# Kernel tuning notes

Measured on AMD Instinct MI355X. Metric: run time of the kernel, lower is better.

The kernel has to match this reference:

```python
import jax, jax.numpy as jnp
import numpy as np

TS = 16      # tile size
ST = 4       # stride
IN = 224     # image size
G = (IN - TS) // ST + 1   # 53 tiles per side
L = G * G                 # 2809 tiles
CH = [3 * L, 3 * L // 4, 3 * L // 16, 3 * L // 4, 3 * L]  # [8427,2106,526,2106,8427]

# torch_dct-style unnormalized DCT-II matrix and its exact inverse (DCT-III based)
_n = np.arange(TS)
_k = np.arange(TS)[:, None]
_C = np.cos(np.pi * (2 * _n[None, :] + 1) * _k / (2 * TS))  # [k, n]
D_DCT = jnp.asarray(2.0 * _C, jnp.float32)                   # dct: y = D @ x
_w = np.ones(TS); _w[0] = 0.5
D_IDCT = jnp.asarray((_C.T * _w[None, :]) / TS, jnp.float32) # idct: x = Dinv @ y

# gather/scatter indices for unfold/fold (constants)
IH = (np.arange(G) * ST)[:, None] + np.arange(TS)[None, :]   # [G, TS]
IW = IH


def setup_inputs() -> dict:
    key = jax.random.key(0)
    ks = jax.random.split(key, 9)
    x = jax.random.normal(ks[0], (8, 3, IN, IN), jnp.float32)
    def lin(k, o, c):
        return jax.random.normal(k, (o, c), jnp.float32) * 0.02
    return {
        'x': x,
        'w1': lin(ks[1], CH[1], CH[0]), 'b1': jnp.zeros((CH[1],), jnp.float32),
        'w2': lin(ks[2], CH[2], CH[1]), 'b2': jnp.zeros((CH[2],), jnp.float32),
        'w3': lin(ks[3], CH[3], CH[2]), 'b3': jnp.zeros((CH[3],), jnp.float32),
        'w4': lin(ks[4], CH[4], CH[3]), 'b4': jnp.zeros((CH[4],), jnp.float32),
    }


def _forward(x, w1, b1, w2, b2, w3, b3, w4, b4):
    b = x.shape[0]
    # unfold: gather overlapping 16x16 patches -> [b, 3, G, G, TS, TS]
    p = x[:, :, IH[:, None, :, None], IW[None, :, None, :]]
    # torch ordering after permute+reshape: channel index = l*3 + c
    tiles = p.transpose(0, 2, 3, 1, 4, 5).reshape(b, 3 * L, TS, TS)
    # 2D DCT (unnormalized DCT-II along last two dims)
    dct_tiles = jnp.einsum('km,ln,bcmn->bckl', D_DCT, D_DCT, tiles)
    # mask net: stack of 1x1 convs over the tile-channel dim
    h = dct_tiles / (TS * TS)
    h = jax.nn.relu(jnp.einsum('oc,bchw->bohw', w1, h) + b1[:, None, None])
    h = jax.nn.relu(jnp.einsum('oc,bchw->bohw', w2, h) + b2[:, None, None])
    h = jax.nn.relu(jnp.einsum('oc,bchw->bohw', w3, h) + b3[:, None, None])
    masks = jax.nn.sigmoid(jnp.einsum('oc,bchw->bohw', w4, h) + b4[:, None, None])
    clean_dct = masks * dct_tiles
    # 2D inverse DCT
    clean_tiles = jnp.einsum('mk,nl,bckl->bcmn', D_IDCT, D_IDCT, clean_dct)
    # fold: scatter-add patches back with overlap
    ct = clean_tiles.reshape(b, G, G, 3, TS, TS).transpose(0, 3, 1, 2, 4, 5)
    out = jnp.zeros((b, 3, IN, IN), x.dtype)
    out = out.at[:, :, IH[:, None, :, None], IW[None, :, None, :]].add(ct)
    # scale = fold(unfold(ones)): per-pixel overlap counts (recomputed per call, as in source)
    scale = jnp.zeros((IN, IN), x.dtype)
    scale = scale.at[IH[:, None, :, None], IW[None, :, None, :]].add(
        jnp.ones((G, G, TS, TS), x.dtype))
    return out / scale


def reference(x, w1, b1, w2, b2, w3, b3, w4, b4):
    return _forward(x, w1, b1, w2, b2, w3, b3, w4, b4)
```

## Files before the change

### kernel.cpp

```cpp
#include <hip/hip_runtime.h>
#include <stdint.h>

constexpr int INSZ = 224;
constexpr int GD   = 53;
constexpr int C0R = 8427, C1R = 2106, C2R = 526;
constexpr int C0P = 8448, C1P = 2304, C2P = 640;
constexpr int NTOK = 2048;

typedef __attribute__((ext_vector_type(4))) float f32x4;
typedef __attribute__((ext_vector_type(8))) short bf16x8;

constexpr float CT[64] = {
  1.00000000f,  0.99518473f,  0.98078528f,  0.95694034f,
  0.92387953f,  0.88192126f,  0.83146961f,  0.77301045f,
  0.70710678f,  0.63439328f,  0.55557023f,  0.47139674f,
  0.38268343f,  0.29028468f,  0.19509032f,  0.09801714f,
  0.00000000f, -0.09801714f, -0.19509032f, -0.29028468f,
 -0.38268343f, -0.47139674f, -0.55557023f, -0.63439328f,
 -0.70710678f, -0.77301045f, -0.83146961f, -0.88192126f,
 -0.92387953f, -0.95694034f, -0.98078528f, -0.99518473f,
 -1.00000000f, -0.99518473f, -0.98078528f, -0.95694034f,
 -0.92387953f, -0.88192126f, -0.83146961f, -0.77301045f,
 -0.70710678f, -0.63439328f, -0.55557023f, -0.47139674f,
 -0.38268343f, -0.29028468f, -0.19509032f, -0.09801714f,
 -0.00000000f,  0.09801714f,  0.19509032f,  0.29028468f,
  0.38268343f,  0.47139674f,  0.55557023f,  0.63439328f,
  0.70710678f,  0.77301045f,  0.83146961f,  0.88192126f,
  0.92387953f,  0.95694034f,  0.98078528f,  0.99518473f
};
constexpr float Dfwd(int k, int n) { return 2.0f * CT[((2 * n + 1) * k) & 63]; }
constexpr float Dinv(int n, int k) { return CT[((2 * n + 1) * k) & 63] * (k == 0 ? 0.03125f : 0.0625f); }

constexpr int TRS_R = 20, TRS_T = 336;
constexpr int TRS_SZ = 15 * TRS_T + 15 * TRS_R + 16;

__device__ __forceinline__ unsigned short f2bf(float f) {
  union { float f; unsigned u; } v; v.f = f;
  return (unsigned short)((v.u + 0x7FFFu + ((v.u >> 16) & 1u)) >> 16);
}
__device__ __forceinline__ float bf2f(unsigned short b) {
  union { unsigned u; float f; } v; v.u = ((unsigned)b) << 16;
  return v.f;
}

__device__ __forceinline__ void gload_lds16(const void* g, void* l) {
  __builtin_amdgcn_global_load_lds(
      (__attribute__((address_space(1))) unsigned int*)(uintptr_t)g,
      (__attribute__((address_space(3))) unsigned int*)(unsigned int)(uintptr_t)l,
      16, 0, 0);
}

__device__ __forceinline__ void xcd_tile(int& bx, int& by) {
  const int gx = gridDim.x, gy = gridDim.y;
  const int nwg = gx * gy;
  const int bid = blockIdx.y * gx + blockIdx.x;
  const int cpx = nwg >> 3;
  const int l = (bid & 7) * cpx + (bid >> 3);
  const int stripe = gy << 2;
  const int bxg = l / stripe;
  const int r = l - bxg * stripe;
  const int rem = gx - (bxg << 2);
  const int w = rem < 4 ? rem : 4;
  by = r / w;
  bx = (bxg << 2) + (r - by * w);
}

constexpr int CV1_GPR = C0P / 8;
constexpr int CV1_TOT = C1P * CV1_GPR;
__global__ __launch_bounds__(256)
void cvt_pad8_w1(const float* __restrict__ src, unsigned short* __restrict__ dst) {
  const int i = blockIdx.x * 256 + threadIdx.x;
  if (i >= CV1_TOT) return;
  const int m = i / CV1_GPR;
  const int k0 = (i - m * CV1_GPR) * 8;
  const float* sr = src + (size_t)m * C0R + k0;
  const bool mok = (m < C1R);
  unsigned short h[8];
#pragma unroll
  for (int e = 0; e < 8; ++e)
    h[e] = f2bf((mok && k0 + e < C0R) ? sr[e] : 0.f);
  uint4 pk;
  pk.x = (unsigned)h[0] | ((unsigned)h[1] << 16);
  pk.y = (unsigned)h[2] | ((unsigned)h[3] << 16);
  pk.z = (unsigned)h[4] | ((unsigned)h[5] << 16);
  pk.w = (unsigned)h[6] | ((unsigned)h[7] << 16);
  *(uint4*)&dst[(size_t)m * C0P + k0] = pk;
}

constexpr int CV8_1 = C2P * C1P / 8;
constexpr int CV8_2 = CV8_1 + C1P * C2P / 8;
constexpr int CV8_T = CV8_2 + C0P * C1P / 8;
__global__ __launch_bounds__(256)
void cvt_pad8_all(const float* __restrict__ w2, const float* __restrict__ w3,
                  const float* __restrict__ w4, unsigned short* __restrict__ d2,
                  unsigned short* __restrict__ d3, unsigned short* __restrict__ d4) {
  const int i = blockIdx.x * 256 + threadIdx.x;
  const float* src; unsigned short* dst;
  int m, k0, Kreal, Mreal, Kp;
  if (i < CV8_1) {
    const int gpr = C1P / 8;
    m = i / gpr; k0 = (i - m * gpr) * 8;
    src = w2; dst = d2; Mreal = C2R; Kreal = C1R; Kp = C1P;
  } else if (i < CV8_2) {
    const int j = i - CV8_1;
    const int gpr = C2P / 8;
    m = j / gpr; k0 = (j - m * gpr) * 8;
    src = w3; dst = d3; Mreal = C1R; Kreal = C2R; Kp = C2P;
  } else {
    const int j = i - CV8_2;
    const int gpr = C1P / 8;
    m = j / gpr; k0 = (j - m * gpr) * 8;
    src = w4; dst = d4; Mreal = C0R; Kreal = C1R; Kp = C1P;
  }
  const float* sr = src + (size_t)m * Kreal + k0;
  const bool mok = (m < Mreal);
  unsigned short h[8];
#pragma unroll
  for (int e = 0; e < 8; ++e)
    h[e] = f2bf((mok && k0 + e < Kreal) ? sr[e] : 0.f);
  uint4 pk;
  pk.x = (unsigned)h[0] | ((unsigned)h[1] << 16);
  pk.y = (unsigned)h[2] | ((unsigned)h[3] << 16);
  pk.z = (unsigned)h[4] | ((unsigned)h[5] << 16);
  pk.w = (unsigned)h[6] | ((unsigned)h[7] << 16);
  *(uint4*)&dst[(size_t)m * Kp + k0] = pk;
}

__global__ __launch_bounds__(256)
void dct_h0(const float* __restrict__ x, unsigned short* __restrict__ H0) {
  __shared__ float trp[TRS_SZ];
  __shared__ unsigned short hst[256 * 64];
  const int tid = threadIdx.x;
  const int b   = blockIdx.y;
  const int c0  = blockIdx.x * 64;
  const int t = tid >> 4, q = tid & 15;

  for (int g = 0; g < 4; ++g) {
    const int c = c0 + g * 16 + t;
    float p[16];
    {
      float4 v0{}, v1{}, v2{}, v3{};
      if (c < C0R) {
        const int ch = c % 3, gw = (c / 3) % GD, gh = c / (3 * GD);
        const float* xr = x + ((size_t)(b * 3 + ch) * INSZ + (gh * 4 + q)) * INSZ + gw * 4;
        v0 = *(const float4*)(xr);      v1 = *(const float4*)(xr + 4);
        v2 = *(const float4*)(xr + 8);  v3 = *(const float4*)(xr + 12);
      }
      p[0]=v0.x; p[1]=v0.y; p[2]=v0.z; p[3]=v0.w;
      p[4]=v1.x; p[5]=v1.y; p[6]=v1.z; p[7]=v1.w;
      p[8]=v2.x; p[9]=v2.y; p[10]=v2.z; p[11]=v2.w;
      p[12]=v3.x; p[13]=v3.y; p[14]=v3.z; p[15]=v3.w;
    }
    float r[16];
#pragma unroll
    for (int k = 0; k < 16; ++k) {
      float s = 0.f;
#pragma unroll
      for (int n = 0; n < 16; ++n) s += p[n] * Dfwd(k, n);
      r[k] = s;
    }
    float* wr = &trp[t * TRS_T + q * TRS_R];
#pragma unroll
    for (int k = 0; k < 16; k += 4)
      *(float4*)(wr + k) = make_float4(r[k], r[k+1], r[k+2], r[k+3]);
    __syncthreads();
    const int j = q;
    float rr[16];
#pragma unroll
    for (int i = 0; i < 16; ++i) rr[i] = trp[t * TRS_T + i * TRS_R + j];
#pragma unroll
    for (int k = 0; k < 16; ++k) {
      float s = 0.f;
#pragma unroll
      for (int i = 0; i < 16; ++i) s += rr[i] * Dfwd(k, i);
      hst[(k * 16 + j) * 64 + g * 16 + t] = f2bf(s * (1.f / 256.f));
    }
    __syncthreads();
  }
  const size_t base = ((size_t)b * 256) * C0P + c0;
#pragma unroll
  for (int i = 0; i < 8; ++i) {
    const int s = i * 256 + tid;
    const int kl = s >> 3, c16 = s & 7;
    *(uint4*)&H0[base + (size_t)kl * C0P + c16 * 8] = *(const uint4*)&hst[kl * 64 + c16 * 8];
  }
}

template<int ACT, int OUT_NM, int SPLITK>
__global__ __launch_bounds__(512, 2)
void gemm256(const unsigned short* __restrict__ W, const unsigned short* __restrict__ Ht,
             const float* __restrict__ bias, void* __restrict__ outp,
             int ldo, int Kp, int chunkK) {
  __shared__ unsigned short As[4][8192];
  __shared__ unsigned short Bs[4][8192];
  int bx, by; xcd_tile(bx, by);
  const int m0 = bx * 256, n0 = by * 256;
  const int tid = threadIdx.x;
  const int w = tid >> 6, lane = tid & 63;
  const int wr = w >> 2, wc = w & 3;
  const int lhi = lane >> 4, llo = lane & 15;
  const int kbase = SPLITK ? blockIdx.z * chunkK : 0;
  const int nkt = chunkK >> 5;

  const int srow = tid >> 2;
  const int slgc = ((tid & 3) ^ ((srow >> 1) & 3)) * 8;

  f32x4 acc[8][4];
#pragma unroll
  for (int i = 0; i < 8; ++i)
#pragma unroll
    for (int j = 0; j < 4; ++j) acc[i][j] = f32x4{0.f, 0.f, 0.f, 0.f};

  auto STAGE_A = [&](int kt, int buf) {
    const int kb = kbase + kt * 32 + slgc;
    gload_lds16(W + (size_t)(m0 + srow) * Kp + kb,       &As[buf][w * 512]);
    gload_lds16(W + (size_t)(m0 + 128 + srow) * Kp + kb, &As[buf][4096 + w * 512]);
  };
  auto STAGE_B = [&](int kt, int buf) {
    const int kb = kbase + kt * 32 + slgc;
    gload_lds16(Ht + (size_t)(n0 + srow) * Kp + kb,       &Bs[buf][w * 512]);
    gload_lds16(Ht + (size_t)(n0 + 128 + srow) * Kp + kb, &Bs[buf][4096 + w * 512]);
  };

  STAGE_A(0, 0); STAGE_B(0, 0);
  if (nkt > 1) { STAGE_A(1, 1); STAGE_B(1, 1); }
  if (nkt > 2) { STAGE_A(2, 2); STAGE_B(2, 2); }
  if (nkt > 2)      asm volatile("s_waitcnt vmcnt(8)" ::: "memory");
  else if (nkt > 1) asm volatile("s_waitcnt vmcnt(4)" ::: "memory");
  else              asm volatile("s_waitcnt vmcnt(0)" ::: "memory");
  __builtin_amdgcn_s_barrier();

  for (int kt = 0; kt < nkt; ++kt) {
    const int buf  = kt & 3;
    const int sbuf = (kt + 3) & 3;
    bf16x8 af[4], bfr[4];
#pragma unroll
    for (int mi = 0; mi < 4; ++mi) {
      const int row = wr * 128 + mi * 16 + llo;
      af[mi] = *(const bf16x8*)(&As[buf][row * 32 + ((lhi ^ ((row >> 1) & 3)) << 3)]);
    }
#pragma unroll
    for (int ni = 0; ni < 4; ++ni) {
      const int row = wc * 64 + ni * 16 + llo;
      bfr[ni] = *(const bf16x8*)(&Bs[buf][row * 32 + ((lhi ^ ((row >> 1) & 3)) << 3)]);
    }
    if (kt + 3 < nkt) STAGE_A(kt + 3, sbuf);
    __builtin_amdgcn_s_barrier();
    asm volatile("s_waitcnt lgkmcnt(0)" ::: "memory");
    __builtin_amdgcn_sched_barrier(0);
    __builtin_amdgcn_s_setprio(1);
#pragma unroll
    for (int mi = 0; mi < 4; ++mi)
#pragma unroll
      for (int ni = 0; ni < 4; ++ni)
        acc[mi][ni] = OUT_NM
          ? __builtin_amdgcn_mfma_f32_16x16x32_bf16(bfr[ni], af[mi], acc[mi][ni], 0, 0, 0)
          : __builtin_amdgcn_mfma_f32_16x16x32_bf16(af[mi], bfr[ni], acc[mi][ni], 0, 0, 0);
    __builtin_amdgcn_s_setprio(0);
    __builtin_amdgcn_s_barrier();
#pragma unroll
    for (int mi = 0; mi < 4; ++mi) {
      const int row = wr * 128 + 64 + mi * 16 + llo;
      af[mi] = *(const bf16x8*)(&As[buf][row * 32 + ((lhi ^ ((row >> 1) & 3)) << 3)]);
    }
    if (kt + 3 < nkt) STAGE_B(kt + 3, sbuf);
    __builtin_amdgcn_s_barrier();
    asm volatile("s_waitcnt lgkmcnt(0)" ::: "memory");
    __builtin_amdgcn_sched_barrier(0);
    __builtin_amdgcn_s_setprio(1);
#pragma unroll
    for (int mi = 0; mi < 4; ++mi)
#pragma unroll
      for (int ni = 0; ni < 4; ++ni)
        acc[4 + mi][ni] = OUT_NM
          ? __builtin_amdgcn_mfma_f32_16x16x32_bf16(bfr[ni], af[mi], acc[4 + mi][ni], 0, 0, 0)
          : __builtin_amdgcn_mfma_f32_16x16x32_bf16(af[mi], bfr[ni], acc[4 + mi][ni], 0, 0, 0);
    __builtin_amdgcn_s_setprio(0);
    if (kt + 1 < nkt) {
      if (kt + 4 <= nkt)      asm volatile("s_waitcnt vmcnt(8)" ::: "memory");
      else if (kt + 3 == nkt) asm volatile("s_waitcnt vmcnt(4)" ::: "memory");
      else                    asm volatile("s_waitcnt vmcnt(0)" ::: "memory");
    }
    __builtin_amdgcn_s_barrier();
  }

  if (SPLITK) {
    float* pz = (float*)outp + (size_t)blockIdx.z * ((size_t)NTOK * ldo);
#pragma unroll
    for (int mh = 0; mh < 2; ++mh)
#pragma unroll
      for (int mi = 0; mi < 4; ++mi) {
        const int mg = m0 + wr * 128 + mh * 64 + mi * 16 + llo;
#pragma unroll
        for (int ni = 0; ni < 4; ++ni) {
          const int ng = n0 + wc * 64 + ni * 16 + lhi * 4;
#pragma unroll
          for (int r = 0; r < 4; ++r)
            pz[(size_t)(ng + r) * ldo + mg] = acc[mh * 4 + mi][ni][r];
        }
      }
  } else {
    unsigned short* out = (unsigned short*)outp;
#pragma unroll
    for (int mh = 0; mh < 2; ++mh)
#pragma unroll
      for (int mi = 0; mi < 4; ++mi) {
        const int mgb = m0 + wr * 128 + mh * 64 + mi * 16 + lhi * 4;
#pragma unroll
        for (int ni = 0; ni < 4; ++ni) {
          const int ng = n0 + wc * 64 + ni * 16 + llo;
#pragma unroll
          for (int r = 0; r < 4; ++r) {
            const int mg = mgb + r;
            float v = acc[mh * 4 + mi][ni][r] + bias[mg];
            if (ACT == 1) v = fmaxf(v, 0.f);
            else if (ACT == 2) v = 1.f / (1.f + expf(-v));
            out[(size_t)mg * ldo + ng] = f2bf(v);
          }
        }
      }
  }
}

template<int OUT_NM>
__device__ __forceinline__ void gemm_core(
    const unsigned short* __restrict__ W, const unsigned short* __restrict__ Ht,
    unsigned short (*As)[128 * 32], unsigned short (*Bs)[128 * 32],
    int m0, int n0, int Kp, int kbase, int nkt, int w, int lane, f32x4 acc[4][4]) {
  const int wr = w >> 1, wc = w & 1;
  const int lhi = lane >> 4, llo = lane & 15;

  const int chunk0 = w * 64 + lane;
  const int row0 = chunk0 >> 2, kc0 = chunk0 & 3;
  const int kcg0 = kc0 ^ ((row0 >> 1) & 3);
  const int chunk1 = 256 + w * 64 + lane;
  const int row1 = chunk1 >> 2, kc1 = chunk1 & 3;
  const int kcg1 = kc1 ^ ((row1 >> 1) & 3);

  auto STAGE = [&](int kt, int sel) {
    const int kb = kbase + kt * 32;
    gload_lds16(W  + (size_t)(m0 + row0) * Kp + kb + kcg0 * 8, &As[sel][(w * 64) * 8]);
    gload_lds16(Ht + (size_t)(n0 + row0) * Kp + kb + kcg0 * 8, &Bs[sel][(w * 64) * 8]);
    gload_lds16(W  + (size_t)(m0 + row1) * Kp + kb + kcg1 * 8, &As[sel][(256 + w * 64) * 8]);
    gload_lds16(Ht + (size_t)(n0 + row1) * Kp + kb + kcg1 * 8, &Bs[sel][(256 + w * 64) * 8]);
  };

  STAGE(0, 0);
  if (nkt > 1) STAGE(1, 1);

  int cur = 0, nxt = 1, nx2 = 2;
  for (int kt = 0; kt < nkt; ++kt) {
    if (kt + 1 < nkt) {
      asm volatile("s_waitcnt vmcnt(4)" ::: "memory");
      __builtin_amdgcn_s_barrier();
      __builtin_amdgcn_sched_barrier(0);
      if (kt + 2 < nkt) STAGE(kt + 2, nx2);
    } else {
      asm volatile("s_waitcnt vmcnt(0)" ::: "memory");
      __builtin_amdgcn_s_barrier();
      __builtin_amdgcn_sched_barrier(0);
    }
    bf16x8 af[4], bfr[4];
#pragma unroll
    for (int mi = 0; mi < 4; ++mi) {
      const int row = wr * 64 + mi * 16 + llo;
      af[mi] = *(const bf16x8*)(&As[cur][row * 32 + (lhi ^ ((row >> 1) & 3)) * 8]);
    }
#pragma unroll
    for (int ni = 0; ni < 4; ++ni) {
      const int row = wc * 64 + ni * 16 + llo;
      bfr[ni] = *(const bf16x8*)(&Bs[cur][row * 32 + (lhi ^ ((row >> 1) & 3)) * 8]);
    }
#pragma unroll
    for (int mi = 0; mi < 4; ++mi)
#pragma unroll
      for (int ni = 0; ni < 4; ++ni) {
        if (OUT_NM)
          acc[mi][ni] = __builtin_amdgcn_mfma_f32_16x16x32_bf16(bfr[ni], af[mi], acc[mi][ni], 0, 0, 0);
        else
          acc[mi][ni] = __builtin_amdgcn_mfma_f32_16x16x32_bf16(af[mi], bfr[ni], acc[mi][ni], 0, 0, 0);
      }
    const int tmp = cur; cur = nxt; nxt = nx2; nx2 = tmp;
  }
}

template<int ACT, int OUT_NM>
__global__ __launch_bounds__(256)
void gemm_bt(const unsigned short* __restrict__ W, const unsigned short* __restrict__ Ht,
             const float* __restrict__ bias, int Mreal,
             unsigned short* __restrict__ out, int ldo, int Kp) {
  __shared__ unsigned short As[3][128 * 32];
  __shared__ unsigned short Bs[3][128 * 32];
  int bx, by; xcd_tile(bx, by);
  const int tid = threadIdx.x;
  const int w = tid >> 6, lane = tid & 63;
  const int m0 = bx * 128, n0 = by * 128;
  const int wr = w >> 1, wc = w & 1;
  const int lhi = lane >> 4, llo = lane & 15;

  f32x4 acc[4][4];
#pragma unroll
  for (int i = 0; i < 4; ++i)
#pragma unroll
    for (int j = 0; j < 4; ++j) acc[i][j] = f32x4{0.f, 0.f, 0.f, 0.f};

  gemm_core<OUT_NM>(W, Ht, As, Bs, m0, n0, Kp, 0, Kp >> 5, w, lane, acc);

  if (OUT_NM) {
#pragma unroll
    for (int mi = 0; mi < 4; ++mi) {
      const int mg = m0 + wr * 64 + mi * 16 + llo;
      const float bv = (mg < Mreal) ? bias[mg] : 0.f;
#pragma unroll
      for (int ni = 0; ni < 4; ++ni) {
        const int ng = n0 + wc * 64 + ni * 16 + lhi * 4;
#pragma unroll
        for (int r = 0; r < 4; ++r) {
          float v = acc[mi][ni][r] + bv;
          if (ACT == 1) v = fmaxf(v, 0.f);
          else if (ACT == 2) v = 1.f / (1.f + expf(-v));
          out[(size_t)(ng + r) * ldo + mg] = f2bf(v);
        }
      }
    }
  } else {
#pragma unroll
    for (int mi = 0; mi < 4; ++mi) {
      const int mgb = m0 + wr * 64 + mi * 16 + lhi * 4;
#pragma unroll
      for (int ni = 0; ni < 4; ++ni) {
        const int ng = n0 + wc * 64 + ni * 16 + llo;
#pragma unroll
        for (int r = 0; r < 4; ++r) {
          const int mg = mgb + r;
          float v = acc[mi][ni][r] + ((mg < Mreal) ? bias[mg] : 0.f);
          if (ACT == 1) v = fmaxf(v, 0.f);
          else if (ACT == 2) v = 1.f / (1.f + expf(-v));
          out[(size_t)mg * ldo + ng] = f2bf(v);
        }
      }
    }
  }
}

__global__ __launch_bounds__(256)
void gemm_splitk(const unsigned short* __restrict__ W, const unsigned short* __restrict__ Ht,
                 float* __restrict__ part, int ldo , int Kp, int chunkK) {
  __shared__ unsigned short As[3][128 * 32];
  __shared__ unsigned short Bs[3][128 * 32];
  int bx, by; xcd_tile(bx, by);
  const int z = blockIdx.z;
  const int tid = threadIdx.x;
  const int w = tid >> 6, lane = tid & 63;
  const int m0 = bx * 128, n0 = by * 128;
  const int wr = w >> 1, wc = w & 1;
  const int lhi = lane >> 4, llo = lane & 15;

  f32x4 acc[4][4];
#pragma unroll
  for (int i = 0; i < 4; ++i)
#pragma unroll
    for (int j = 0; j < 4; ++j) acc[i][j] = f32x4{0.f, 0.f, 0.f, 0.f};

  gemm_core<1>(W, Ht, As, Bs, m0, n0, Kp, z * chunkK, chunkK >> 5, w, lane, acc);

  float* pz = part + (size_t)z * NTOK * ldo;
#pragma unroll
  for (int mi = 0; mi < 4; ++mi) {
    const int mg = m0 + wr * 64 + mi * 16 + llo;
#pragma unroll
    for (int ni = 0; ni < 4; ++ni) {
      const int ng = n0 + wc * 64 + ni * 16 + lhi * 4;
#pragma unroll
      for (int r = 0; r < 4; ++r)
        pz[(size_t)(ng + r) * ldo + mg] = acc[mi][ni][r];
    }
  }
}

__global__ __launch_bounds__(256)
void reduce_act(const float* __restrict__ part, const float* __restrict__ bias,
                unsigned short* __restrict__ out, int Mp, int Mreal, int nch) {
  const int i8 = blockIdx.x * 256 + threadIdx.x;
  const int total = NTOK * Mp / 8;
  if (i8 >= total) return;
  const size_t off = (size_t)i8 * 8;
  const int m0 = (int)(off % Mp);
  float s[8] = {0.f, 0.f, 0.f, 0.f, 0.f, 0.f, 0.f, 0.f};
  for (int z = 0; z < nch; ++z) {
    const float4 v0 = *(const float4*)(part + (size_t)z * NTOK * Mp + off);
    const float4 v1 = *(const float4*)(part + (size_t)z * NTOK * Mp + off + 4);
    s[0] += v0.x; s[1] += v0.y; s[2] += v0.z; s[3] += v0.w;
    s[4] += v1.x; s[5] += v1.y; s[6] += v1.z; s[7] += v1.w;
  }
  unsigned short h[8];
#pragma unroll
  for (int e = 0; e < 8; ++e) {
    const float b = (m0 + e < Mreal) ? bias[m0 + e] : 0.f;
    h[e] = f2bf(fmaxf(s[e] + b, 0.f));
  }
  uint4 pk;
  pk.x = (unsigned)h[0] | ((unsigned)h[1] << 16);
  pk.y = (unsigned)h[2] | ((unsigned)h[3] << 16);
  pk.z = (unsigned)h[4] | ((unsigned)h[5] << 16);
  pk.w = (unsigned)h[6] | ((unsigned)h[7] << 16);
  *(uint4*)&out[off] = pk;
}

__global__ __launch_bounds__(256)
void mask_idct(const float* __restrict__ x, const unsigned short* __restrict__ masks,
               unsigned short* __restrict__ clean) {
  __shared__ float trp[TRS_SZ];
  const int tid = threadIdx.x;
  const int b   = blockIdx.y;
  const int c0  = blockIdx.x * 16;
  const int t = tid >> 4, q = tid & 15;
  const int c = c0 + t;
  const bool valid = (c < C0R);

  float p[16];
  {
    float4 v0{}, v1{}, v2{}, v3{};
    if (valid) {
      const int ch = c % 3, gw = (c / 3) % GD, gh = c / (3 * GD);
      const float* xr = x + ((size_t)(b * 3 + ch) * INSZ + (gh * 4 + q)) * INSZ + gw * 4;
      v0 = *(const float4*)(xr);      v1 = *(const float4*)(xr + 4);
      v2 = *(const float4*)(xr + 8);  v3 = *(const float4*)(xr + 12);
    }
    p[0]=v0.x; p[1]=v0.y; p[2]=v0.z; p[3]=v0.w;
    p[4]=v1.x; p[5]=v1.y; p[6]=v1.z; p[7]=v1.w;
    p[8]=v2.x; p[9]=v2.y; p[10]=v2.z; p[11]=v2.w;
    p[12]=v3.x; p[13]=v3.y; p[14]=v3.z; p[15]=v3.w;
  }
  float r[16];
#pragma unroll
  for (int k = 0; k < 16; ++k) {
    float s = 0.f;
#pragma unroll
    for (int n = 0; n < 16; ++n) s += p[n] * Dfwd(k, n);
    r[k] = s;
  }
  {
    float* wr = &trp[t * TRS_T + q * TRS_R];
#pragma unroll
    for (int k = 0; k < 16; k += 4)
      *(float4*)(wr + k) = make_float4(r[k], r[k+1], r[k+2], r[k+3]);
  }
  __syncthreads();
  const int j = q;
  float rr[16];
#pragma unroll
  for (int i = 0; i < 16; ++i) rr[i] = trp[t * TRS_T + i * TRS_R + j];
  float cd[16];
  const unsigned short* mrow = masks + (size_t)c * NTOK + (size_t)b * 256 + j;
#pragma unroll
  for (int k = 0; k < 16; ++k) {
    float s = 0.f;
#pragma unroll
    for (int i = 0; i < 16; ++i) s += rr[i] * Dfwd(k, i);
    const float mv = valid ? bf2f(mrow[k * 16]) : 0.f;
    cd[k] = s * mv;
  }
  float t3[16];
#pragma unroll
  for (int m = 0; m < 16; ++m) {
    float s = 0.f;
#pragma unroll
    for (int k = 0; k < 16; ++k) s += cd[k] * Dinv(m, k);
    t3[m] = s;
  }
  __syncthreads();
  {
    float* wr = &trp[t * TRS_T + j * TRS_R];
#pragma unroll
    for (int m = 0; m < 16; m += 4)
      *(float4*)(wr + m) = make_float4(t3[m], t3[m+1], t3[m+2], t3[m+3]);
  }
  __syncthreads();
  float tr[16];
#pragma unroll
  for (int l = 0; l < 16; ++l) tr[l] = trp[t * TRS_T + l * TRS_R + q];
  if (valid) {
    unsigned pk[8];
#pragma unroll
    for (int n2 = 0; n2 < 8; ++n2) {
      float s0 = 0.f, s1 = 0.f;
#pragma unroll
      for (int l = 0; l < 16; ++l) {
        s0 += tr[l] * Dinv(2 * n2, l);
        s1 += tr[l] * Dinv(2 * n2 + 1, l);
      }
      pk[n2] = (unsigned)f2bf(s0) | ((unsigned)f2bf(s1) << 16);
    }
    unsigned short* dst = clean + ((size_t)b * C0R + c) * 256 + q * 16;
    uint4* d4 = (uint4*)dst;
    d4[0] = make_uint4(pk[0], pk[1], pk[2], pk[3]);
    d4[1] = make_uint4(pk[4], pk[5], pk[6], pk[7]);
  }
}

__global__ void overlap_add(const unsigned short* __restrict__ clean, float* __restrict__ out) {
  const int px = blockIdx.x * 256 + threadIdx.x;
  if (px >= 8 * 3 * 224 * 224) return;
  const int j = px % 224;
  const int i = (px / 224) % 224;
  const int bc = px / (224 * 224);
  const int ch = bc % 3, b = bc / 3;
  const int ilo = i - 15;
  const int ghlo = ilo > 0 ? (ilo + 3) >> 2 : 0;
  const int ghhi = (i >> 2) < 52 ? (i >> 2) : 52;
  const int jlo = j - 15;
  const int gwlo = jlo > 0 ? (jlo + 3) >> 2 : 0;
  const int gwhi = (j >> 2) < 52 ? (j >> 2) : 52;
  float sum = 0.f;
  for (int gh = ghlo; gh <= ghhi; ++gh) {
    const int r = i - gh * 4;
    const size_t base = ((size_t)b * C0R + (size_t)gh * (3 * GD) + ch) * 256 + (size_t)r * 16 + j;
    for (int gw = gwlo; gw <= gwhi; ++gw) {
      sum += bf2f(clean[base + (size_t)gw * 764]);
    }
  }
  const int cnt = (ghhi - ghlo + 1) * (gwhi - gwlo + 1);
  out[px] = sum / (float)cnt;
}

extern "C" void kernel_launch(void* const* d_in, const int* in_sizes, int n_in,
                              void* d_out, int out_size, void* d_ws, size_t ws_size,
                              hipStream_t stream) {
  const float* x  = (const float*)d_in[0];
  const float* w1 = (const float*)d_in[1];
  const float* b1 = (const float*)d_in[2];
  const float* w2 = (const float*)d_in[3];
  const float* b2 = (const float*)d_in[4];
  const float* w3 = (const float*)d_in[5];
  const float* b3 = (const float*)d_in[6];
  const float* w4 = (const float*)d_in[7];
  const float* b4 = (const float*)d_in[8];
  float* out = (float*)d_out;
  char* ws = (char*)d_ws;

  const size_t OFF_A = 0;
  const size_t OFF_B = 38928384;
  const size_t OFF_C = 73531392;

  unsigned short* wb1   = (unsigned short*)(ws + OFF_A);
  unsigned short* wb4   = (unsigned short*)(ws + OFF_A);
  unsigned short* clean = (unsigned short*)(ws + OFF_A);

  unsigned short* H0v = (unsigned short*)(ws + OFF_B);
  unsigned short* Y1  = (unsigned short*)(ws + OFF_B);
  unsigned short* wb2 = (unsigned short*)(ws + OFF_B + 9437184);
  unsigned short* wb3 = (unsigned short*)(ws + OFF_B + 12386304);
  unsigned short* Y2  = (unsigned short*)(ws + OFF_B + 15335424);
  unsigned short* msk = (unsigned short*)(ws + OFF_B);

  float* pt1 = (float*)(ws + OFF_C);
  float* pt2 = (float*)(ws + OFF_C);
  float* pt3 = (float*)(ws + OFF_C);
  unsigned short* Y3 = (unsigned short*)(ws + OFF_C + 37748736);

  cvt_pad8_w1<<<dim3(CV1_TOT / 256), 256, 0, stream>>>(w1, wb1);
  dct_h0<<<dim3(C0P / 64, 8), 256, 0, stream>>>(x, H0v);

  gemm256<0, 1, 1><<<dim3(C1P / 256, NTOK / 256, 3), 512, 0, stream>>>(
      wb1, H0v, nullptr, pt1, C1P, C0P, 2816);
  reduce_act<<<dim3(NTOK * C1P / 8 / 256), 256, 0, stream>>>(pt1, b1, Y1, C1P, C1R, 3);

  cvt_pad8_all<<<dim3(CV8_T / 256), 256, 0, stream>>>(w2, w3, w4, wb2, wb3, wb4);

  gemm_splitk<<<dim3(C2P / 128, NTOK / 128, 4), 256, 0, stream>>>(wb2, Y1, pt2, C2P, C1P, 576);
  reduce_act<<<dim3(NTOK * C2P / 8 / 256), 256, 0, stream>>>(pt2, b2, Y2, C2P, C2R, 4);

  gemm_splitk<<<dim3(C1P / 128, NTOK / 128, 2), 256, 0, stream>>>(wb3, Y2, pt3, C1P, C2P, 320);
  reduce_act<<<dim3(NTOK * C1P / 8 / 256), 256, 0, stream>>>(pt3, b3, Y3, C1P, C1R, 2);

  gemm256<2, 0, 0><<<dim3(32, NTOK / 256), 512, 0, stream>>>(
      wb4, Y3, b4, msk, NTOK, C1P, C1P);
  gemm_bt<2, 0><<<dim3(2, NTOK / 128), 256, 0, stream>>>(
      wb4 + (size_t)8192 * C1P, Y3, b4 + 8192, C0R - 8192,
      msk + (size_t)8192 * NTOK, NTOK, C1P);

  mask_idct<<<dim3((C0R + 15) / 16, 8), 256, 0, stream>>>(x, msk, clean);

  overlap_add<<<dim3((8 * 3 * 224 * 224 + 255) / 256), 256, 0, stream>>>(clean, out);
}
```

Baseline: 445.0 us.

## Split-K the tail mask GEMM and restructure gemm256 barrier pipeline

After: 403.3 us. -9.4%, faster.

```diff
diff --git a/kernel.cpp b/kernel.cpp
--- a/kernel.cpp
+++ b/kernel.cpp
@@ -225,14 +225,16 @@
   STAGE_A(0, 0); STAGE_B(0, 0);
   if (nkt > 1) { STAGE_A(1, 1); STAGE_B(1, 1); }
   if (nkt > 2) { STAGE_A(2, 2); STAGE_B(2, 2); }
-  if (nkt > 2)      asm volatile("s_waitcnt vmcnt(8)" ::: "memory");
-  else if (nkt > 1) asm volatile("s_waitcnt vmcnt(4)" ::: "memory");
-  else              asm volatile("s_waitcnt vmcnt(0)" ::: "memory");
-  __builtin_amdgcn_s_barrier();
 
   for (int kt = 0; kt < nkt; ++kt) {
     const int buf  = kt & 3;
     const int sbuf = (kt + 3) & 3;
+    if (kt + 3 <= nkt)      asm volatile("s_waitcnt vmcnt(8)" ::: "memory");
+    else if (kt + 2 == nkt) asm volatile("s_waitcnt vmcnt(4)" ::: "memory");
+    else                    asm volatile("s_waitcnt vmcnt(0)" ::: "memory");
+    __builtin_amdgcn_s_barrier();
+    __builtin_amdgcn_sched_barrier(0);
+
     bf16x8 af[4], bfr[4];
 #pragma unroll
     for (int mi = 0; mi < 4; ++mi) {
@@ -245,9 +247,6 @@
       bfr[ni] = *(const bf16x8*)(&Bs[buf][row * 32 + ((lhi ^ ((row >> 1) & 3)) << 3)]);
     }
     if (kt + 3 < nkt) STAGE_A(kt + 3, sbuf);
-    __builtin_amdgcn_s_barrier();
-    asm volatile("s_waitcnt lgkmcnt(0)" ::: "memory");
-    __builtin_amdgcn_sched_barrier(0);
     __builtin_amdgcn_s_setprio(1);
 #pragma unroll
     for (int mi = 0; mi < 4; ++mi)
@@ -257,16 +256,12 @@
           ? __builtin_amdgcn_mfma_f32_16x16x32_bf16(bfr[ni], af[mi], acc[mi][ni], 0, 0, 0)
           : __builtin_amdgcn_mfma_f32_16x16x32_bf16(af[mi], bfr[ni], acc[mi][ni], 0, 0, 0);
     __builtin_amdgcn_s_setprio(0);
-    __builtin_amdgcn_s_barrier();
 #pragma unroll
     for (int mi = 0; mi < 4; ++mi) {
       const int row = wr * 128 + 64 + mi * 16 + llo;
       af[mi] = *(const bf16x8*)(&As[buf][row * 32 + ((lhi ^ ((row >> 1) & 3)) << 3)]);
     }
     if (kt + 3 < nkt) STAGE_B(kt + 3, sbuf);
-    __builtin_amdgcn_s_barrier();
-    asm volatile("s_waitcnt lgkmcnt(0)" ::: "memory");
-    __builtin_amdgcn_sched_barrier(0);
     __builtin_amdgcn_s_setprio(1);
 #pragma unroll
     for (int mi = 0; mi < 4; ++mi)
@@ -276,12 +271,6 @@
           ? __builtin_amdgcn_mfma_f32_16x16x32_bf16(bfr[ni], af[mi], acc[4 + mi][ni], 0, 0, 0)
           : __builtin_amdgcn_mfma_f32_16x16x32_bf16(af[mi], bfr[ni], acc[4 + mi][ni], 0, 0, 0);
     __builtin_amdgcn_s_setprio(0);
-    if (kt + 1 < nkt) {
-      if (kt + 4 <= nkt)      asm volatile("s_waitcnt vmcnt(8)" ::: "memory");
-      else if (kt + 3 == nkt) asm volatile("s_waitcnt vmcnt(4)" ::: "memory");
-      else                    asm volatile("s_waitcnt vmcnt(0)" ::: "memory");
-    }
-    __builtin_amdgcn_s_barrier();
   }
 
   if (SPLITK) {
@@ -384,65 +373,6 @@
   }
 }
 
-template<int ACT, int OUT_NM>
-__global__ __launch_bounds__(256)
-void gemm_bt(const unsigned short* __restrict__ W, const unsigned short* __restrict__ Ht,
-             const float* __restrict__ bias, int Mreal,
-             unsigned short* __restrict__ out, int ldo, int Kp) {
-  __shared__ unsigned short As[3][128 * 32];
-  __shared__ unsigned short Bs[3][128 * 32];
-  int bx, by; xcd_tile(bx, by);
-  const int tid = threadIdx.x;
-  const int w = tid >> 6, lane = tid & 63;
-  const int m0 = bx * 128, n0 = by * 128;
-  const int wr = w >> 1, wc = w & 1;
-  const int lhi = lane >> 4, llo = lane & 15;
-
-  f32x4 acc[4][4];
-#pragma unroll
-  for (int i = 0; i < 4; ++i)
-#pragma unroll
-    for (int j = 0; j < 4; ++j) acc[i][j] = f32x4{0.f, 0.f, 0.f, 0.f};
-
-  gemm_core<OUT_NM>(W, Ht, As, Bs, m0, n0, Kp, 0, Kp >> 5, w, lane, acc);
-
-  if (OUT_NM) {
-#pragma unroll
-    for (int mi = 0; mi < 4; ++mi) {
-      const int mg = m0 + wr * 64 + mi * 16 + llo;
-      const float bv = (mg < Mreal) ? bias[mg] : 0.f;
-#pragma unroll
-      for (int ni = 0; ni < 4; ++ni) {
-        const int ng = n0 + wc * 64 + ni * 16 + lhi * 4;
-#pragma unroll
-        for (int r = 0; r < 4; ++r) {
-          float v = acc[mi][ni][r] + bv;
-          if (ACT == 1) v = fmaxf(v, 0.f);
-          else if (ACT == 2) v = 1.f / (1.f + expf(-v));
-          out[(size_t)(ng + r) * ldo + mg] = f2bf(v);
-        }
-      }
-    }
-  } else {
-#pragma unroll
-    for (int mi = 0; mi < 4; ++mi) {
-      const int mgb = m0 + wr * 64 + mi * 16 + lhi * 4;
-#pragma unroll
-      for (int ni = 0; ni < 4; ++ni) {
-        const int ng = n0 + wc * 64 + ni * 16 + llo;
-#pragma unroll
-        for (int r = 0; r < 4; ++r) {
-          const int mg = mgb + r;
-          float v = acc[mi][ni][r] + ((mg < Mreal) ? bias[mg] : 0.f);
-          if (ACT == 1) v = fmaxf(v, 0.f);
-          else if (ACT == 2) v = 1.f / (1.f + expf(-v));
-          out[(size_t)mg * ldo + ng] = f2bf(v);
-        }
-      }
-    }
-  }
-}
-
 __global__ __launch_bounds__(256)
 void gemm_splitk(const unsigned short* __restrict__ W, const unsigned short* __restrict__ Ht,
                  float* __restrict__ part, int ldo , int Kp, int chunkK) {
@@ -476,6 +406,71 @@
         pz[(size_t)(ng + r) * ldo + mg] = acc[mi][ni][r];
     }
   }
+}
+
+__global__ __launch_bounds__(256)
+void gemm_splitk_mn(const unsigned short* __restrict__ W, const unsigned short* __restrict__ Ht,
+                    float* __restrict__ part, int Kp, int chunkK) {
+  __shared__ unsigned short As[3][128 * 32];
+  __shared__ unsigned short Bs[3][128 * 32];
+  int bx, by; xcd_tile(bx, by);
+  const int z = blockIdx.z;
+  const int tid = threadIdx.x;
+  const int w = tid >> 6, lane = tid & 63;
+  const int m0 = bx * 128, n0 = by * 128;
+  const int wr = w >> 1, wc = w & 1;
+  const int lhi = lane >> 4, llo = lane & 15;
+  const int Mloc = gridDim.x * 128;
+
+  f32x4 acc[4][4];
+#pragma unroll
+  for (int i = 0; i < 4; ++i)
+#pragma unroll
+    for (int j = 0; j < 4; ++j) acc[i][j] = f32x4{0.f, 0.f, 0.f, 0.f};
+
+  gemm_core<0>(W, Ht, As, Bs, m0, n0, Kp, z * chunkK, chunkK >> 5, w, lane, acc);
+
+  float* pz = part + (size_t)z * Mloc * NTOK;
+#pragma unroll
+  for (int mi = 0; mi < 4; ++mi) {
+    const int mlb = m0 + wr * 64 + mi * 16 + lhi * 4;
+#pragma unroll
+    for (int ni = 0; ni < 4; ++ni) {
+      const int ng = n0 + wc * 64 + ni * 16 + llo;
+#pragma unroll
+      for (int r = 0; r < 4; ++r)
+        pz[(size_t)(mlb + r) * NTOK + ng] = acc[mi][ni][r];
+    }
+  }
+}
+
+__global__ __launch_bounds__(256)
+void reduce_sig(const float* __restrict__ part, const float* __restrict__ bias,
+                unsigned short* __restrict__ msk, int mbase, int Mloc, int nch) {
+  const int i8 = blockIdx.x * 256 + threadIdx.x;
+  const int total = Mloc * NTOK / 8;
+  if (i8 >= total) return;
+  const size_t off = (size_t)i8 * 8;
+  const int ml = (int)(off >> 11);
+  float s[8] = {0.f, 0.f, 0.f, 0.f, 0.f, 0.f, 0.f, 0.f};
+  for (int z = 0; z < nch; ++z) {
+    const float4 v0 = *(const float4*)(part + (size_t)z * Mloc * NTOK + off);
+    const float4 v1 = *(const float4*)(part + (size_t)z * Mloc * NTOK + off + 4);
+    s[0] += v0.x; s[1] += v0.y; s[2] += v0.z; s[3] += v0.w;
+    s[4] += v1.x; s[5] += v1.y; s[6] += v1.z; s[7] += v1.w;
+  }
+  const int mg = mbase + ml;
+  const float b = (mg < C0R) ? bias[mg] : 0.f;
+  unsigned short h[8];
+#pragma unroll
+  for (int e = 0; e < 8; ++e)
+    h[e] = f2bf(1.f / (1.f + expf(-(s[e] + b))));
+  uint4 pk;
+  pk.x = (unsigned)h[0] | ((unsigned)h[1] << 16);
+  pk.y = (unsigned)h[2] | ((unsigned)h[3] << 16);
+  pk.z = (unsigned)h[4] | ((unsigned)h[5] << 16);
+  pk.w = (unsigned)h[6] | ((unsigned)h[7] << 16);
+  *(uint4*)&msk[(size_t)mg * NTOK + (off & 2047)] = pk;
 }
 
 __global__ __launch_bounds__(256)
@@ -657,6 +652,7 @@
   float* pt1 = (float*)(ws + OFF_C);
   float* pt2 = (float*)(ws + OFF_C);
   float* pt3 = (float*)(ws + OFF_C);
+  float* pt4 = (float*)(ws + OFF_C);
   unsigned short* Y3 = (unsigned short*)(ws + OFF_C + 37748736);
 
   cvt_pad8_w1<<<dim3(CV1_TOT / 256), 256, 0, stream>>>(w1, wb1);
@@ -676,9 +672,9 @@
 
   gemm256<2, 0, 0><<<dim3(32, NTOK / 256), 512, 0, stream>>>(
       wb4, Y3, b4, msk, NTOK, C1P, C1P);
-  gemm_bt<2, 0><<<dim3(2, NTOK / 128), 256, 0, stream>>>(
-      wb4 + (size_t)8192 * C1P, Y3, b4 + 8192, C0R - 8192,
-      msk + (size_t)8192 * NTOK, NTOK, C1P);
+  gemm_splitk_mn<<<dim3(2, NTOK / 128, 4), 256, 0, stream>>>(
+      wb4 + (size_t)8192 * C1P, Y3, pt4, C1P, 576);
+  reduce_sig<<<dim3(256 * NTOK / 8 / 256), 256, 0, stream>>>(pt4, b4, msk, 8192, 256, 4);
 
   mask_idct<<<dim3((C0R + 15) / 16, 8), 256, 0, stream>>>(x, msk, clean);
 
```
